# Kernel optimization log

Measured on AMD Instinct MI355X. Metric: run time of the kernel, lower is better.

Reference implementation:

```python
import jax, jax.numpy as jnp
import numpy as np

B, S, D, F_, E, K = 64, 8, 2048, 4096, 8, 2


def setup_inputs() -> dict:
    key = jax.random.key(0)
    ks = jax.random.split(key, 5)
    scale_in = 1.0 / np.sqrt(D)
    scale_ff = 1.0 / np.sqrt(F_)
    return {
        "x": jax.random.normal(ks[0], (B, S, D), dtype=jnp.float32),
        "gate_w": jax.random.normal(ks[1], (D, E), dtype=jnp.float32) * scale_in,
        "w1": jax.random.normal(ks[2], (E, D, F_), dtype=jnp.float32) * scale_in,
        "w3": jax.random.normal(ks[3], (E, D, F_), dtype=jnp.float32) * scale_in,
        "w2": jax.random.normal(ks[4], (E, F_, D), dtype=jnp.float32) * scale_ff,
        "top_k": K,
    }


def reference(x, gate_w, w1, w3, w2, top_k):
    # x: [B,S,D]; gate_w: [D,E]; w1,w3: [E,D,F]; w2: [E,F,D]
    n_experts = gate_w.shape[-1]
    gate_logits = jnp.einsum("bsd,de->bse", x, gate_w)          # [B,S,E]
    weights, selected = jax.lax.top_k(gate_logits, top_k)        # [B,S,K]
    weights = jax.nn.softmax(weights, axis=-1)                   # softmax over k (dim=2)
    # per-token combine weight for every expert: [B,S,E]
    combine = jnp.einsum(
        "bsk,bske->bse", weights, jax.nn.one_hot(selected, n_experts, dtype=x.dtype)
    )
    # SwiGLU expert FFN, batched over the (small, fixed) expert axis
    h = jax.nn.silu(jnp.einsum("bsd,edf->ebsf", x, w1)) * jnp.einsum(
        "bsd,edf->ebsf", x, w3
    )                                                            # [E,B,S,F]
    expert_out = jnp.einsum("ebsf,efd->ebsd", h, w2)             # [E,B,S,D]
    return jnp.einsum("bse,ebsd->bsd", combine, expert_out)      # [B,S,D]
```

## Files before the change

### kernel.cpp

```cpp
#include <hip/hip_runtime.h>
#include <hip/hip_bf16.h>
#include <cstdint>
#include <cstddef>

#define NB   64
#define NS   8
#define DIM  2048
#define FF   4096
#define NE   8
#define TOK  512
#define NPAIR 1024

#define BM   192
#define BKE  32
#define ASZ  (BM * 4 * 8)

typedef __attribute__((ext_vector_type(4))) float f32x4;
typedef __attribute__((ext_vector_type(8))) short bf16x8;

#define MFMA16(a, b, c) __builtin_amdgcn_mfma_f32_16x16x32_bf16((a), (b), (c), 0, 0, 0)
#define SCHEDBAR __builtin_amdgcn_sched_barrier(0)
#define LGKMBAR do { asm volatile("s_waitcnt lgkmcnt(0)" ::: "memory"); \
                     asm volatile("s_barrier" ::: "memory");            \
                     __builtin_amdgcn_sched_barrier(0); } while (0)

static __device__ __forceinline__ short f2bf(float f) {
    unsigned u = __builtin_bit_cast(unsigned, f);
    return (short)((u + 0x8000u) >> 16);
}
static __device__ __forceinline__ unsigned cvtpk(float lo, float hi) {
    unsigned r;
    asm("v_cvt_pk_bf16_f32 %0, %1, %2" : "=v"(r) : "v"(lo), "v"(hi));
    return r;
}
static __device__ __forceinline__ bf16x8 pack8(const float* v) {
    uint4 u;
    u.x = cvtpk(v[0], v[1]); u.y = cvtpk(v[2], v[3]);
    u.z = cvtpk(v[4], v[5]); u.w = cvtpk(v[6], v[7]);
    return __builtin_bit_cast(bf16x8, u);
}

static __device__ __forceinline__ void async16(void* l, const void* g) {
    __builtin_amdgcn_global_load_lds(
        (const __attribute__((address_space(1))) void*)g,
        (__attribute__((address_space(3))) void*)l, 16, 0, 0);
}

__global__ void gate_topk(const float* __restrict__ x, const float* __restrict__ gw,
                          unsigned short* __restrict__ xbf,
                          int* __restrict__ tok_expert, float* __restrict__ tok_gatew) {
    int token = blockIdx.x;
    int lane  = threadIdx.x;
    const float* xr = x + (size_t)token * DIM;

    float acc[NE];
#pragma unroll
    for (int e = 0; e < NE; ++e) acc[e] = 0.f;

    for (int d0 = lane * 8; d0 < DIM; d0 += 64 * 8) {
        float4 xa = *(const float4*)(xr + d0);
        float4 xb = *(const float4*)(xr + d0 + 4);
        bf16x8 v;
        v[0] = f2bf(xa.x); v[1] = f2bf(xa.y); v[2] = f2bf(xa.z); v[3] = f2bf(xa.w);
        v[4] = f2bf(xb.x); v[5] = f2bf(xb.y); v[6] = f2bf(xb.z); v[7] = f2bf(xb.w);
        *(bf16x8*)(xbf + (size_t)token * DIM + d0) = v;
#pragma unroll
        for (int j = 0; j < 8; ++j) {
            float xv = (j < 4) ? ((const float*)&xa)[j] : ((const float*)&xb)[j - 4];
            const float4* g = (const float4*)(gw + (size_t)(d0 + j) * NE);
            float4 g0 = g[0], g1 = g[1];
            acc[0] += xv * g0.x; acc[1] += xv * g0.y;
            acc[2] += xv * g0.z; acc[3] += xv * g0.w;
            acc[4] += xv * g1.x; acc[5] += xv * g1.y;
            acc[6] += xv * g1.z; acc[7] += xv * g1.w;
        }
    }
#pragma unroll
    for (int off = 32; off >= 1; off >>= 1) {
#pragma unroll
        for (int e = 0; e < NE; ++e) acc[e] += __shfl_down(acc[e], off);
    }
    if (lane == 0) {
        float b1 = -1e30f, b2 = -1e30f; int i1 = 0, i2 = 0;
#pragma unroll
        for (int e = 0; e < NE; ++e) {
            float v = acc[e];
            if (v > b1) { b2 = b1; i2 = i1; b1 = v; i1 = e; }
            else if (v > b2) { b2 = v; i2 = e; }
        }
        float t = __expf(b2 - b1);
        tok_expert[token * 2 + 0] = i1;
        tok_expert[token * 2 + 1] = i2;
        tok_gatew[token * 2 + 0] = 1.f / (1.f + t);
        tok_gatew[token * 2 + 1] = t / (1.f + t);
    }
}

__global__ void build_lists(const int* __restrict__ tok_expert,
                            const float* __restrict__ tok_gatew,
                            int* __restrict__ counts, int* __restrict__ offsets,
                            int* __restrict__ row_token, float* __restrict__ row_gatew,
                            int* __restrict__ pair_row) {
    __shared__ int s_off[NE];
    __shared__ int s_cnt[NE];
    int e    = threadIdx.x >> 6;
    int lane = threadIdx.x & 63;
    unsigned long long lt = (1ull << lane) - 1ull;

    int cnt = 0;
    for (int base = 0; base < NPAIR; base += 64) {
        int id = tok_expert[base + lane];
        unsigned long long m = __ballot(id == e);
        cnt += __popcll(m);
    }
    if (lane == 0) s_cnt[e] = cnt;
    __syncthreads();
    if (threadIdx.x == 0) {
        int o = 0;
        for (int i = 0; i < NE; ++i) {
            int c = s_cnt[i];
            counts[i] = c; offsets[i] = o; s_off[i] = o; o += c;
        }
    }
    __syncthreads();

    int rbase = s_off[e];
    for (int base = 0; base < NPAIR; base += 64) {
        int entry = base + lane;
        int id = tok_expert[entry];
        bool match = (id == e);
        unsigned long long m = __ballot(match);
        int pre = __popcll(m & lt);
        if (match) {
            int row = rbase + pre;
            row_token[row] = entry >> 1;
            row_gatew[row] = tok_gatew[entry];
            pair_row[entry] = row;
        }
        rbase += __popcll(m);
    }
}

#define EP1(RD, WR, BSR, BSW, PACKV, LOADV, S, HAS_P, HAS_W) do {           \
    if (HAS_P) {                                                            \
        if (t < 768) async16(&(WR)[(size_t)t * 8], asrc0 + ((S) + 2) * BKE);\
    }                                                                       \
    SCHEDBAR;                                                               \
    if (HAS_P) {                                                            \
        _Pragma("unroll")                                                   \
        for (int j = 0; j < 8; ++j)                                         \
            LOADV[j] = bsrc[(size_t)(((S) + 2) * BKE + j) * FF];            \
    }                                                                       \
    SCHEDBAR;                                                               \
    bf16x8 a_[3];                                                           \
    _Pragma("unroll")                                                       \
    for (int f = 0; f < 3; ++f) {                                           \
        int r_ = wm * 48 + f * 16 + l15;                                    \
        int p_ = (lg + (r_ >> 1)) & 3;                                      \
        a_[f] = *(const bf16x8*)&(RD)[((size_t)r_ * 4 + p_) * 8];           \
    }                                                                       \
    _Pragma("unroll")                                                       \
    for (int nf = 0; nf < 2; ++nf) {                                        \
        int ch_ = wn * 32 + nf * 16 + l15 + lg * 128;                       \
        bf16x8 b1f = *(const bf16x8*)&Bs[BSR][0][ch_][0];                   \
        bf16x8 b3f = *(const bf16x8*)&Bs[BSR][1][ch_][0];                   \
        _Pragma("unroll")                                                   \
        for (int f = 0; f < 3; ++f) {                                       \
            acc1[f][nf] = MFMA16(a_[f], b1f, acc1[f][nf]);                  \
            acc3[f][nf] = MFMA16(a_[f], b3f, acc3[f][nf]);                  \
        }                                                                   \
    }                                                                       \
    if (HAS_W) {                                                            \
        bf16x8 wv = pack8(PACKV);                                           \
        *(bf16x8*)&Bs[BSW][bmat][bch][0] = wv;                              \
    }                                                                       \
    LGKMBAR;                                                                \
} while (0)

__global__ __launch_bounds__(1024, 4) void ffn1(
    const unsigned short* __restrict__ xbf, const float* __restrict__ w1,
    const float* __restrict__ w3,
    const int* __restrict__ counts, const int* __restrict__ offsets,
    const int* __restrict__ row_token, unsigned short* __restrict__ Hbuf) {
    __shared__ __align__(16) unsigned short As[3 * ASZ];
    __shared__ __align__(16) unsigned short Bs[2][2][512][8];

    int bid = blockIdx.x;
    int e  = bid & 7;
    int f0 = (bid >> 3) * 128;

    int Me = counts[e];
    if (Me == 0) return;
    int off = offsets[e];

    int t = threadIdx.x;
    int lane = t & 63;
    int w = t >> 6;
    int wm = w >> 2, wn = w & 3;
    int l15 = lane & 15, lg = lane >> 4;

    const float* w1e = w1 + (size_t)e * DIM * FF + f0;
    const float* w3e = w3 + (size_t)e * DIM * FF + f0;

    int bmat = t >> 9;
    int bc   = t & 511;
    int bcol = bc & 127, blg = bc >> 7;
    const float* bsrc = (bmat ? w3e : w1e) + (size_t)(blg * 8) * FF + bcol;
    int bch = bcol + blg * 128;

    const int NST = DIM / BKE;

    for (int mb = 0; mb < Me; mb += BM) {
        __syncthreads();
        const unsigned short* asrc0 = xbf;
        {
            int m0 = t >> 2, c0 = t & 3;
            int rl0 = mb + m0;
            int tok0 = row_token[off + ((rl0 < Me) ? rl0 : (Me - 1))];
            asrc0 = xbf + (size_t)tok0 * DIM + (((c0 - (m0 >> 1)) & 3) << 3);
        }

        f32x4 acc1[3][2], acc3[3][2];
#pragma unroll
        for (int f = 0; f < 3; ++f)
#pragma unroll
            for (int nf = 0; nf < 2; ++nf) {
                acc1[f][nf] = (f32x4){0.f, 0.f, 0.f, 0.f};
                acc3[f][nf] = (f32x4){0.f, 0.f, 0.f, 0.f};
            }

        unsigned short* pRd = As;
        unsigned short* pMd = As + ASZ;
        unsigned short* pWr = As + 2 * ASZ;

        float bX[8], bY[8];

        if (t < 768) {
            async16(&pRd[(size_t)t * 8], asrc0);
            async16(&pMd[(size_t)t * 8], asrc0 + BKE);
        }
        SCHEDBAR;
#pragma unroll
        for (int j = 0; j < 8; ++j) bX[j] = bsrc[(size_t)j * FF];
        {
            bf16x8 wv = pack8(bX);
            *(bf16x8*)&Bs[0][bmat][bch][0] = wv;
        }
#pragma unroll
        for (int j = 0; j < 8; ++j) bY[j] = bsrc[(size_t)(BKE + j) * FF];
        LGKMBAR;

        for (int s = 0; s < NST - 2; s += 2) {
            EP1(pRd, pWr, 0, 1, bY, bX, s,     1, 1);
            EP1(pMd, pRd, 1, 0, bX, bY, s + 1, 1, 1);
            unsigned short* tt = pRd; pRd = pWr; pWr = pMd; pMd = tt;
        }
        EP1(pRd, pWr, 0, 1, bY, bX, NST - 2, 0, 1);
        EP1(pMd, pRd, 1, 0, bX, bY, NST - 1, 0, 0);

#pragma unroll
        for (int f = 0; f < 3; ++f)
#pragma unroll
            for (int nf = 0; nf < 2; ++nf)
#pragma unroll
                for (int r = 0; r < 4; ++r) {
                    int rl = mb + wm * 48 + f * 16 + lg * 4 + r;
                    if (rl < Me) {
                        float a1 = acc1[f][nf][r], a3 = acc3[f][nf][r];
                        float h = (a1 / (1.f + __expf(-a1))) * a3;
                        Hbuf[(size_t)(off + rl) * FF + f0 + wn * 32 + nf * 16 + l15] =
                            (unsigned short)f2bf(h);
                    }
                }
    }
}

#define EP2(RD, WR, BSR, BSW, PACKV, LOADV, S, HAS_P, HAS_W) do {           \
    if (HAS_P) {                                                            \
        async16(&(WR)[(size_t)t * 8], asrc0 + ((S) + 2) * BKE);             \
        if (t < 256)                                                        \
            async16(&(WR)[(size_t)(512 + t) * 8], asrc1 + ((S) + 2) * BKE); \
    }                                                                       \
    SCHEDBAR;                                                               \
    if (HAS_P) {                                                            \
        _Pragma("unroll")                                                   \
        for (int j = 0; j < 4; ++j)                                         \
            LOADV[j] = bsrc[(size_t)(((S) + 2) * BKE + j) * DIM];           \
    }                                                                       \
    SCHEDBAR;                                                               \
    bf16x8 a_[3];                                                           \
    _Pragma("unroll")                                                       \
    for (int f = 0; f < 3; ++f) {                                           \
        int r_ = wm * 48 + f * 16 + l15;                                    \
        int p_ = (lg + (r_ >> 1)) & 3;                                      \
        a_[f] = *(const bf16x8*)&(RD)[((size_t)r_ * 4 + p_) * 8];           \
    }                                                                       \
    _Pragma("unroll")                                                       \
    for (int nf = 0; nf < 2; ++nf) {                                        \
        int ch_ = wn * 32 + nf * 16 + l15 + lg * 64;                        \
        bf16x8 bw = *(const bf16x8*)&Bs[BSR][ch_][0];                       \
        _Pragma("unroll")                                                   \
        for (int f = 0; f < 3; ++f)                                         \
            acc[f][nf] = MFMA16(a_[f], bw, acc[f][nf]);                     \
    }                                                                       \
    if (HAS_W) {                                                            \
        uint2 u_;                                                           \
        u_.x = cvtpk(PACKV[0], PACKV[1]);                                   \
        u_.y = cvtpk(PACKV[2], PACKV[3]);                                   \
        *(uint2*)&Bs[BSW][bch][bhalf * 4] = u_;                             \
    }                                                                       \
    LGKMBAR;                                                                \
} while (0)

__global__ __launch_bounds__(512, 4) void ffn2(
    const unsigned short* __restrict__ Hbuf, const float* __restrict__ w2,
    const int* __restrict__ counts, const int* __restrict__ offsets,
    const float* __restrict__ row_gatew,
    float* __restrict__ OPa, float* __restrict__ OPb) {
    __shared__ __align__(16) unsigned short As[3 * ASZ];
    __shared__ __align__(16) unsigned short Bs[2][256][8];

    int bid = blockIdx.x;
    int e   = bid & 7;
    int idx = bid >> 3;
    int d0 = (idx >> 1) * 64;
    int ks = idx & 1;
    int k0 = ks * (FF / 2);
    float* OP = ks ? OPb : OPa;

    int Me = counts[e];
    if (Me == 0) return;
    int off = offsets[e];

    int t = threadIdx.x;
    int lane = t & 63;
    int w = t >> 6;
    int wm = w >> 1, wn = w & 1;
    int l15 = lane & 15, lg = lane >> 4;

    const float* w2e = w2 + (size_t)e * FF * DIM + d0;

    int bcol = t & 63, blg = (t >> 6) & 3, bhalf = t >> 8;
    const float* bsrc = w2e + (size_t)(k0 + blg * 8 + bhalf * 4) * DIM + bcol;
    int bch = bcol + blg * 64;

    const int NST = (FF / 2) / BKE;

    for (int mb = 0; mb < Me; mb += BM) {
        __syncthreads();
        const unsigned short* asrc0;
        const unsigned short* asrc1;
        {
            int m0 = t >> 2, c0 = t & 3;
            int rl0 = mb + m0;
            asrc0 = Hbuf + (size_t)(off + ((rl0 < Me) ? rl0 : (Me - 1))) * FF
                         + k0 + (((c0 - (m0 >> 1)) & 3) << 3);
            int i1 = 512 + t;
            int m1 = i1 >> 2, c1 = i1 & 3;
            int rl1 = mb + m1;
            asrc1 = Hbuf + (size_t)(off + ((rl1 < Me) ? rl1 : (Me - 1))) * FF
                         + k0 + (((c1 - (m1 >> 1)) & 3) << 3);
        }

        f32x4 acc[3][2];
#pragma unroll
        for (int f = 0; f < 3; ++f)
#pragma unroll
            for (int nf = 0; nf < 2; ++nf) acc[f][nf] = (f32x4){0.f, 0.f, 0.f, 0.f};

        unsigned short* pRd = As;
        unsigned short* pMd = As + ASZ;
        unsigned short* pWr = As + 2 * ASZ;

        float bX[4], bY[4];

        async16(&pRd[(size_t)t * 8], asrc0);
        if (t < 256) async16(&pRd[(size_t)(512 + t) * 8], asrc1);
        async16(&pMd[(size_t)t * 8], asrc0 + BKE);
        if (t < 256) async16(&pMd[(size_t)(512 + t) * 8], asrc1 + BKE);
        SCHEDBAR;
#pragma unroll
        for (int j = 0; j < 4; ++j) bX[j] = bsrc[(size_t)j * DIM];
        {
            uint2 u_;
            u_.x = cvtpk(bX[0], bX[1]);
            u_.y = cvtpk(bX[2], bX[3]);
            *(uint2*)&Bs[0][bch][bhalf * 4] = u_;
        }
#pragma unroll
        for (int j = 0; j < 4; ++j) bY[j] = bsrc[(size_t)(BKE + j) * DIM];
        LGKMBAR;

        for (int s = 0; s < NST - 2; s += 2) {
            EP2(pRd, pWr, 0, 1, bY, bX, s,     1, 1);
            EP2(pMd, pRd, 1, 0, bX, bY, s + 1, 1, 1);
            unsigned short* tt = pRd; pRd = pWr; pWr = pMd; pMd = tt;
        }
        EP2(pRd, pWr, 0, 1, bY, bX, NST - 2, 0, 1);
        EP2(pMd, pRd, 1, 0, bX, bY, NST - 1, 0, 0);

#pragma unroll
        for (int f = 0; f < 3; ++f)
#pragma unroll
            for (int nf = 0; nf < 2; ++nf)
#pragma unroll
                for (int r = 0; r < 4; ++r) {
                    int rl = mb + wm * 48 + f * 16 + lg * 4 + r;
                    if (rl < Me) {
                        int grow = off + rl;
                        float g = row_gatew[grow];
                        OP[(size_t)grow * DIM + d0 + wn * 32 + nf * 16 + l15] =
                            acc[f][nf][r] * g;
                    }
                }
    }
}

__global__ void combine(const float* __restrict__ OPa, const float* __restrict__ OPb,
                        const int* __restrict__ pair_row, float* __restrict__ out) {
    int idx = blockIdx.x * blockDim.x + threadIdx.x;
    int token = idx >> 9;
    int q = idx & 511;
    int r0 = pair_row[token * 2 + 0];
    int r1 = pair_row[token * 2 + 1];
    float4 a0 = *(const float4*)(OPa + (size_t)r0 * DIM + q * 4);
    float4 b0 = *(const float4*)(OPb + (size_t)r0 * DIM + q * 4);
    float4 a1 = *(const float4*)(OPa + (size_t)r1 * DIM + q * 4);
    float4 b1 = *(const float4*)(OPb + (size_t)r1 * DIM + q * 4);
    float4 o;
    o.x = (a0.x + b0.x) + (a1.x + b1.x);
    o.y = (a0.y + b0.y) + (a1.y + b1.y);
    o.z = (a0.z + b0.z) + (a1.z + b1.z);
    o.w = (a0.w + b0.w) + (a1.w + b1.w);
    *(float4*)(out + (size_t)token * DIM + q * 4) = o;
}

extern "C" void kernel_launch(void* const* d_in, const int* in_sizes, int n_in,
                              void* d_out, int out_size, void* d_ws, size_t ws_size,
                              hipStream_t stream) {
    const float* x  = (const float*)d_in[0];
    const float* gw = (const float*)d_in[1];
    const float* w1 = (const float*)d_in[2];
    const float* w3 = (const float*)d_in[3];
    const float* w2 = (const float*)d_in[4];
    float* out = (float*)d_out;

    char* ws = (char*)d_ws;
    unsigned short* Hbuf = (unsigned short*)ws;
    float* OPa           = (float*)(ws + 8388608);
    unsigned short* xbf  = (unsigned short*)(ws + 16777216);
    float* OPb           = (float*)(ws + 20971520);
    char* meta           = ws + 29360128;
    int*   tok_expert = (int*)(meta);
    float* tok_gatew  = (float*)(meta + 4096);
    int*   counts     = (int*)(meta + 8192);
    int*   offsets    = (int*)(meta + 8224);
    int*   row_token  = (int*)(meta + 8256);
    float* row_gatew  = (float*)(meta + 12352);
    int*   pair_row   = (int*)(meta + 16448);

    gate_topk<<<TOK, 64, 0, stream>>>(x, gw, xbf, tok_expert, tok_gatew);
    build_lists<<<1, 512, 0, stream>>>(tok_expert, tok_gatew, counts, offsets,
                                       row_token, row_gatew, pair_row);
    ffn1<<<NE * 32, 1024, 0, stream>>>(xbf, w1, w3, counts, offsets, row_token, Hbuf);
    ffn2<<<NE * 64, 512, 0, stream>>>(Hbuf, w2, counts, offsets, row_gatew, OPa, OPb);
    combine<<<1024, 256, 0, stream>>>(OPa, OPb, pair_row, out);
}
```

Measured before the change: 198.4 us.

## Split ffn1 reduction dimension in two with partial sums and merge kernel

Doubles ffn1's grid by splitting the D reduction into two halves. Each half writes fp32 partial accumulators for w1 and w3 to workspace buffers. A new merge kernel sums the partials, applies SiLU-gating and writes bf16 H. The aim is more blocks across CUs to hide latency in the weight-streaming GEMM, at the cost of extra fp32 traffic (about 64MB written and read) and one more launch.

```diff
diff --git a/kernel.cpp b/kernel.cpp
--- a/kernel.cpp
+++ b/kernel.cpp
@@ -181,13 +181,20 @@
     const unsigned short* __restrict__ xbf, const float* __restrict__ w1,
     const float* __restrict__ w3,
     const int* __restrict__ counts, const int* __restrict__ offsets,
-    const int* __restrict__ row_token, unsigned short* __restrict__ Hbuf) {
+    const int* __restrict__ row_token,
+    float* __restrict__ P1a, float* __restrict__ P1b,
+    float* __restrict__ P3a, float* __restrict__ P3b) {
     __shared__ __align__(16) unsigned short As[3 * ASZ];
     __shared__ __align__(16) unsigned short Bs[2][2][512][8];
 
     int bid = blockIdx.x;
-    int e  = bid & 7;
-    int f0 = (bid >> 3) * 128;
+    int e   = bid & 7;
+    int idx = bid >> 3;
+    int f0 = (idx >> 1) * 128;
+    int ks = idx & 1;
+    int k0 = ks * (DIM / 2);
+    float* P1 = ks ? P1b : P1a;
+    float* P3 = ks ? P3b : P3a;
 
     int Me = counts[e];
     if (Me == 0) return;
@@ -205,10 +212,10 @@
     int bmat = t >> 9;
     int bc   = t & 511;
     int bcol = bc & 127, blg = bc >> 7;
-    const float* bsrc = (bmat ? w3e : w1e) + (size_t)(blg * 8) * FF + bcol;
+    const float* bsrc = (bmat ? w3e : w1e) + (size_t)(k0 + blg * 8) * FF + bcol;
     int bch = bcol + blg * 128;
 
-    const int NST = DIM / BKE;
+    const int NST = (DIM / 2) / BKE;
 
     for (int mb = 0; mb < Me; mb += BM) {
         __syncthreads();
@@ -217,7 +224,7 @@
             int m0 = t >> 2, c0 = t & 3;
             int rl0 = mb + m0;
             int tok0 = row_token[off + ((rl0 < Me) ? rl0 : (Me - 1))];
-            asrc0 = xbf + (size_t)tok0 * DIM + (((c0 - (m0 >> 1)) & 3) << 3);
+            asrc0 = xbf + (size_t)tok0 * DIM + k0 + (((c0 - (m0 >> 1)) & 3) << 3);
         }
 
         f32x4 acc1[3][2], acc3[3][2];
@@ -266,13 +273,33 @@
                 for (int r = 0; r < 4; ++r) {
                     int rl = mb + wm * 48 + f * 16 + lg * 4 + r;
                     if (rl < Me) {
-                        float a1 = acc1[f][nf][r], a3 = acc3[f][nf][r];
-                        float h = (a1 / (1.f + __expf(-a1))) * a3;
-                        Hbuf[(size_t)(off + rl) * FF + f0 + wn * 32 + nf * 16 + l15] =
-                            (unsigned short)f2bf(h);
+                        size_t o = (size_t)(off + rl) * FF + f0 + wn * 32 + nf * 16 + l15;
+                        P1[o] = acc1[f][nf][r];
+                        P3[o] = acc3[f][nf][r];
                     }
                 }
     }
+}
+
+__global__ void ffn1_merge(const float* __restrict__ P1a, const float* __restrict__ P1b,
+                           const float* __restrict__ P3a, const float* __restrict__ P3b,
+                           unsigned short* __restrict__ Hbuf) {
+    size_t i = ((size_t)blockIdx.x * blockDim.x + threadIdx.x) * 4;
+    float4 a1a = *(const float4*)(P1a + i);
+    float4 a1b = *(const float4*)(P1b + i);
+    float4 a3a = *(const float4*)(P3a + i);
+    float4 a3b = *(const float4*)(P3b + i);
+    float h[4];
+#pragma unroll
+    for (int j = 0; j < 4; ++j) {
+        float a1 = ((const float*)&a1a)[j] + ((const float*)&a1b)[j];
+        float a3 = ((const float*)&a3a)[j] + ((const float*)&a3b)[j];
+        h[j] = (a1 / (1.f + __expf(-a1))) * a3;
+    }
+    uint2 u;
+    u.x = cvtpk(h[0], h[1]);
+    u.y = cvtpk(h[2], h[3]);
+    *(uint2*)(Hbuf + i) = u;
 }
 
 #define EP2(RD, WR, BSR, BSW, PACKV, LOADV, S, HAS_P, HAS_W) do {           \
@@ -450,7 +477,11 @@
     float* OPa           = (float*)(ws + 8388608);
     unsigned short* xbf  = (unsigned short*)(ws + 16777216);
     float* OPb           = (float*)(ws + 20971520);
-    char* meta           = ws + 29360128;
+    float* P1a           = (float*)(ws + 33554432);
+    float* P1b           = (float*)(ws + 50331648);
+    float* P3a           = (float*)(ws + 67108864);
+    float* P3b           = (float*)(ws + 83886080);
+    char* meta           = ws + 100663296;
     int*   tok_expert = (int*)(meta);
     float* tok_gatew  = (float*)(meta + 4096);
     int*   counts     = (int*)(meta + 8192);
@@ -462,7 +493,9 @@
     gate_topk<<<TOK, 64, 0, stream>>>(x, gw, xbf, tok_expert, tok_gatew);
     build_lists<<<1, 512, 0, stream>>>(tok_expert, tok_gatew, counts, offsets,
                                        row_token, row_gatew, pair_row);
-    ffn1<<<NE * 32, 1024, 0, stream>>>(xbf, w1, w3, counts, offsets, row_token, Hbuf);
+    ffn1<<<NE * 64, 1024, 0, stream>>>(xbf, w1, w3, counts, offsets, row_token,
+                                       P1a, P1b, P3a, P3b);
+    ffn1_merge<<<(NPAIR * FF) / (4 * 256), 256, 0, stream>>>(P1a, P1b, P3a, P3b, Hbuf);
     ffn2<<<NE * 64, 512, 0, stream>>>(Hbuf, w2, counts, offsets, row_gatew, OPa, OPb);
     combine<<<1024, 256, 0, stream>>>(OPa, OPb, pair_row, out);
 }
```

Measured after the change: 232.9 us. 1.17x slower.
